# Kernel tuning notes

Measured on AMD Instinct MI355X. Metric: run time of the kernel, lower is better.

Reference implementation:

```python
import jax, jax.numpy as jnp
import numpy as np

B, T, D = 2, 2048, 1024
H, HKV, HD = 16, 4, 64  # num_heads, num_kv_heads, head_dim
EPS = 1.1920929e-07  # torch.finfo(float32).eps, nn.RMSNorm default


def _rmsnorm(x, g):
    return x * jax.lax.rsqrt(jnp.mean(x * x, axis=-1, keepdims=True) + EPS) * g


def _ternary(w):
    # ternary quantize {-1,0,+1} with straight-through estimator
    th = jnp.mean(jnp.abs(w))
    wt = jnp.sign(w) * (jnp.abs(w) > th).astype(w.dtype)
    return w + jax.lax.stop_gradient(wt - w)


def _bitlinear(x, w, g):
    return _rmsnorm(x, g) @ _ternary(w).T


def setup_inputs() -> dict:
    key = jax.random.key(0)
    ks = jax.random.split(key, 5)
    kaiming = lambda k, shape: jax.random.normal(k, shape, jnp.float32) * np.float32(np.sqrt(2.0 / shape[1]))
    return {
        "x": jax.random.normal(ks[0], (B, T, D), jnp.float32),
        "q_w": kaiming(ks[1], (D, D)),
        "q_g": jnp.ones((D,), jnp.float32),
        "k_w": kaiming(ks[2], (HKV * HD, D)),
        "k_g": jnp.ones((D,), jnp.float32),
        "v_w": kaiming(ks[3], (HKV * HD, D)),
        "o_w": kaiming(ks[4], (D, D)),
        "o_g": jnp.ones((D,), jnp.float32),
        "qk_gain": jnp.float32(5.25),
    }


def reference(x, q_w, q_g, k_w, k_g, v_w, o_w, o_g, qk_gain):
    b, t, d = x.shape
    q = _bitlinear(x, q_w, q_g).reshape(b, t, H, HD)          # [B,T,H,hd]
    k = _bitlinear(x, k_w, k_g).reshape(b, t, HKV, HD)        # [B,T,Hkv,hd]
    v = (x @ v_w.T).reshape(b, t, HKV, HD)                    # [B,T,Hkv,hd]
    rep = H // HKV
    k = jnp.repeat(k, rep, axis=2)                            # GQA expand -> [B,T,H,hd]
    v = jnp.repeat(v, rep, axis=2)
    scale = qk_gain / np.float32(np.sqrt(HD))
    attn = jnp.einsum('bqhd,bkhd->bhqk', q, k) * scale        # [B,H,T,T]
    causal = jnp.tril(jnp.ones((t, t), bool))
    attn = jnp.where(causal, attn, -jnp.inf)
    attn = jax.nn.softmax(attn, axis=-1)
    out = jnp.einsum('bhqk,bkhd->bqhd', attn, v).reshape(b, t, d)
    return _bitlinear(out, o_w, o_g)
```

## Files before the change

kernel.cpp:

```cpp
#include <hip/hip_runtime.h>
#include <hip/hip_bf16.h>
#include <cstdint>
#include <cstddef>

typedef unsigned short u16;
typedef unsigned int u32;
typedef __attribute__((ext_vector_type(8))) short short8v;
typedef __attribute__((ext_vector_type(4))) float f32x4;
typedef __attribute__((ext_vector_type(4))) u16 u16x4;
typedef __attribute__((ext_vector_type(8))) u16 u16x8;

static constexpr int Bc = 2, Tc = 2048, Dc = 1024, Hc = 16, HKVc = 4, HDc = 64;
static constexpr int Mc = Bc * Tc;
static constexpr float EPSc = 1.1920929e-07f;

static __device__ __forceinline__ u16 f2bf(float f) {
  u32 u = __builtin_bit_cast(u32, f);
  return (u16)((u + 0x7fffu + ((u >> 16) & 1u)) >> 16);
}
static __device__ __forceinline__ float bf2f(u16 b) {
  u32 u = ((u32)b) << 16;
  return __builtin_bit_cast(float, u);
}
static __device__ __forceinline__ float fast_exp2(float x) {
  float r;
  asm("v_exp_f32 %0, %1" : "=v"(r) : "v"(x));
  return r;
}
static __device__ __forceinline__ u32 cvt_pk_bf16(float lo, float hi) {
  u32 r;
  asm("v_cvt_pk_bf16_f32 %0, %1, %2" : "=v"(r) : "v"(lo), "v"(hi));
  return r;
}

__global__ __launch_bounds__(256) void np_leafsum_all(const float* __restrict__ q_w,
                                                      const float* __restrict__ k_w,
                                                      const float* __restrict__ o_w,
                                                      float* __restrict__ leaf) {
  int blk = blockIdx.x;
  const float* w;
  float* out;
  int lfbase;
  if (blk < 256)      { w = q_w; out = leaf;         lfbase = blk * 32; }
  else if (blk < 320) { w = k_w; out = leaf + 8192;  lfbase = (blk - 256) * 32; }
  else                { w = o_w; out = leaf + 10240; lfbase = (blk - 320) * 32; }
  int t = threadIdx.x;
  int lf = lfbase + (t >> 3), j = t & 7;
  const float* a = w + (size_t)lf * 128;
  float r = fabsf(a[j]);
#pragma unroll
  for (int i = 8; i < 128; i += 8) r += fabsf(a[i + j]);
  float x = r + __shfl_xor(r, 1);
  float y = x + __shfl_xor(x, 2);
  float z = y + __shfl_xor(y, 4);
  if (j == 0) out[lf] = z;
}

__global__ __launch_bounds__(256) void np_treemean3(const float* __restrict__ leaf,
                                                    float* __restrict__ th) {
  int m = blockIdx.x;
  const float* src = leaf + (m == 0 ? 0 : (m == 1 ? 8192 : 10240));
  int nle = (m == 1) ? 2048 : 8192;
  float inv_n = (m == 1) ? (1.0f / 262144.0f) : (1.0f / 1048576.0f);
  int t = threadIdx.x;
  int chunk = nle >> 8;
  float v[32];
  for (int i = 0; i < chunk; i += 4) {
    float4 f = *(const float4*)&src[t * chunk + i];
    v[i] = f.x; v[i + 1] = f.y; v[i + 2] = f.z; v[i + 3] = f.w;
  }
  for (int cnt = chunk >> 1; cnt >= 1; cnt >>= 1)
    for (int i = 0; i < cnt; ++i) v[i] = v[2 * i] + v[2 * i + 1];
  float s = v[0];
#pragma unroll
  for (int off = 1; off < 64; off <<= 1) s += __shfl_xor(s, off);
  __shared__ float red[4];
  if ((t & 63) == 0) red[t >> 6] = s;
  __syncthreads();
  if (t == 0) th[m] = ((red[0] + red[1]) + (red[2] + red[3])) * inv_n;
}

__global__ __launch_bounds__(256) void quant_split_all(const float* __restrict__ q_w,
                                                       const float* __restrict__ k_w,
                                                       const float* __restrict__ o_w,
                                                       const float* __restrict__ v_w,
                                                       const float* __restrict__ th,
                                                       u16* __restrict__ Wq,
                                                       u16* __restrict__ Wk,
                                                       u16* __restrict__ Wo,
                                                       u16* __restrict__ Vwh) {
  int i4 = blockIdx.x * 256 + threadIdx.x;
  if (i4 < 589824) {
    const float* w; u16* o; float t;
    int j;
    if (i4 < 262144)      { w = q_w; o = Wq; t = th[0]; j = i4; }
    else if (i4 < 327680) { w = k_w; o = Wk; t = th[1]; j = i4 - 262144; }
    else                  { w = o_w; o = Wo; t = th[2]; j = i4 - 327680; }
    float4 v = *(const float4*)&w[(size_t)j * 4];
    float y[4] = {v.x, v.y, v.z, v.w};
    u16x4 q;
#pragma unroll
    for (int c = 0; c < 4; ++c)
      q[c] = (y[c] > t) ? (u16)0x3F80 : ((y[c] < -t) ? (u16)0xBF80 : (u16)0);
    *(u16x4*)&o[(size_t)j * 4] = q;
  } else {
    int j = i4 - 589824;
    float4 v = *(const float4*)&v_w[(size_t)j * 4];
    float y[4] = {v.x, v.y, v.z, v.w};
    u16x4 h;
#pragma unroll
    for (int c = 0; c < 4; ++c) h[c] = f2bf(y[c]);
    *(u16x4*)&Vwh[(size_t)j * 4] = h;
  }
}

__global__ __launch_bounds__(256) void rmsnorm_split6(const float* __restrict__ X,
                                                      const float* __restrict__ g1,
                                                      const float* __restrict__ g2,
                                                      u16* __restrict__ H1, u16* __restrict__ L1,
                                                      u16* __restrict__ H2, u16* __restrict__ L2,
                                                      u16* __restrict__ HV) {
  int row = blockIdx.x;
  const float* xr = X + (size_t)row * Dc;
  int tid = threadIdx.x;
  float4 v = *(const float4*)&xr[tid * 4];
  float vv[4] = {v.x, v.y, v.z, v.w};
  if (HV != nullptr) {
    u16x4 h;
#pragma unroll
    for (int j = 0; j < 4; ++j) h[j] = f2bf(vv[j]);
    *(u16x4*)&HV[(size_t)row * Dc + tid * 4] = h;
  }
  float ss = v.x * v.x + v.y * v.y + v.z * v.z + v.w * v.w;
#pragma unroll
  for (int off = 1; off < 64; off <<= 1) ss += __shfl_xor(ss, off);
  __shared__ float red[4];
  if ((tid & 63) == 0) red[tid >> 6] = ss;
  __syncthreads();
  float tot = red[0] + red[1] + red[2] + red[3];
  float inv = 1.0f / sqrtf(tot * (1.0f / (float)Dc) + EPSc);
  {
    float4 a = *(const float4*)&g1[tid * 4];
    float ga[4] = {a.x, a.y, a.z, a.w};
    u16x4 h, l;
#pragma unroll
    for (int j = 0; j < 4; ++j) {
      float y = vv[j] * inv * ga[j];
      u16 hb = f2bf(y);
      h[j] = hb;
      l[j] = f2bf(y - bf2f(hb));
    }
    *(u16x4*)&H1[(size_t)row * Dc + tid * 4] = h;
    if (L1 != nullptr) *(u16x4*)&L1[(size_t)row * Dc + tid * 4] = l;
  }
  if (g2 != nullptr) {
    float4 a = *(const float4*)&g2[tid * 4];
    float ga[4] = {a.x, a.y, a.z, a.w};
    u16x4 h, l;
#pragma unroll
    for (int j = 0; j < 4; ++j) {
      float y = vv[j] * inv * ga[j];
      u16 hb = f2bf(y);
      h[j] = hb;
      l[j] = f2bf(y - bf2f(hb));
    }
    *(u16x4*)&H2[(size_t)row * Dc + tid * 4] = h;
    if (L2 != nullptr) *(u16x4*)&L2[(size_t)row * Dc + tid * 4] = l;
  }
}

template <bool PA, bool PB, int MODE, int MF, int NF>
__global__ __launch_bounds__(256, 1) void gemm_mfma(
    const u16* __restrict__ Ah, const u16* __restrict__ Al,
    const u16* __restrict__ Bh, const u16* __restrict__ Bl,
    int M, int N, int K,
    float* __restrict__ C, u16* __restrict__ O1, u16* __restrict__ O2) {
  constexpr int BM = MF * 32, BN = NF * 32;
  constexpr int APT = BM / 32;
  constexpr int BPT = BN / 32;
  __shared__ __align__(16) u16 AhS[BM * 64];
  __shared__ __align__(16) u16 AlS[PA ? BM * 64 : 8];
  __shared__ __align__(16) u16 BhS[BN * 64];
  __shared__ __align__(16) u16 BlS[PB ? BN * 64 : 8];
  int tid = threadIdx.x;
  int l = tid & 63, w = tid >> 6;
  int wm = (w >> 1) * (BM / 2), wn = (w & 1) * (BN / 2);
  int bm = blockIdx.y * BM, bn = blockIdx.x * BN;
  u16x8 rAh[APT], rAl[PA ? APT : 1], rBh[BPT], rBl[PB ? BPT : 1];
  f32x4 acc[MF][NF] = {};
#define LOADTILE(kb_)                                                               \
  {                                                                                 \
    _Pragma("unroll") for (int p = 0; p < APT; ++p) {                               \
      int idx = tid + p * 256;                                                      \
      int row = idx >> 3, cc = idx & 7;                                             \
      rAh[p] = *(const u16x8*)&Ah[(size_t)(bm + row) * K + (kb_) + cc * 8];         \
      if (PA) rAl[p] = *(const u16x8*)&Al[(size_t)(bm + row) * K + (kb_) + cc * 8]; \
    }                                                                               \
    _Pragma("unroll") for (int p = 0; p < BPT; ++p) {                               \
      int idx = tid + p * 256;                                                      \
      int row = idx >> 3, cc = idx & 7;                                             \
      rBh[p] = *(const u16x8*)&Bh[(size_t)(bn + row) * K + (kb_) + cc * 8];         \
      if (PB) rBl[p] = *(const u16x8*)&Bl[(size_t)(bn + row) * K + (kb_) + cc * 8]; \
    }                                                                               \
  }
  LOADTILE(0)
  for (int kb = 0; kb < K; kb += 64) {
    __syncthreads();
#pragma unroll
    for (int p = 0; p < APT; ++p) {
      int idx = tid + p * 256;
      int row = idx >> 3, cc = idx & 7;
      int off = row * 64 + ((cc * 8) ^ ((row & 7) << 3));
      *(u16x8*)&AhS[off] = rAh[p];
      if (PA) *(u16x8*)&AlS[off] = rAl[p];
    }
#pragma unroll
    for (int p = 0; p < BPT; ++p) {
      int idx = tid + p * 256;
      int row = idx >> 3, cc = idx & 7;
      int off = row * 64 + ((cc * 8) ^ ((row & 7) << 3));
      *(u16x8*)&BhS[off] = rBh[p];
      if (PB) *(u16x8*)&BlS[off] = rBl[p];
    }
    if (kb + 64 < K) LOADTILE(kb + 64)
    __syncthreads();
    __builtin_amdgcn_s_setprio(1);
#pragma unroll
    for (int sl = 0; sl < 2; ++sl) {
      short8v fa[MF], fal[MF], fb[NF], fbl[NF];
      int kof = (l >> 4) * 8 + sl * 32;
#pragma unroll
      for (int m = 0; m < MF; ++m) {
        int row = wm + m * 16 + (l & 15);
        int off = row * 64 + (kof ^ ((row & 7) << 3));
        fa[m] = *(const short8v*)&AhS[off];
        if (PA) fal[m] = *(const short8v*)&AlS[off];
      }
#pragma unroll
      for (int n = 0; n < NF; ++n) {
        int row = wn + n * 16 + (l & 15);
        int off = row * 64 + (kof ^ ((row & 7) << 3));
        fb[n] = *(const short8v*)&BhS[off];
        if (PB) fbl[n] = *(const short8v*)&BlS[off];
      }
#pragma unroll
      for (int m = 0; m < MF; ++m)
#pragma unroll
        for (int n = 0; n < NF; ++n) {
          acc[m][n] = __builtin_amdgcn_mfma_f32_16x16x32_bf16(fa[m], fb[n], acc[m][n], 0, 0, 0);
          if (PA)
            acc[m][n] = __builtin_amdgcn_mfma_f32_16x16x32_bf16(fal[m], fb[n], acc[m][n], 0, 0, 0);
          if (PB)
            acc[m][n] = __builtin_amdgcn_mfma_f32_16x16x32_bf16(fa[m], fbl[n], acc[m][n], 0, 0, 0);
        }
    }
    __builtin_amdgcn_s_setprio(0);
  }
#undef LOADTILE
#pragma unroll
  for (int m = 0; m < MF; ++m)
#pragma unroll
    for (int n = 0; n < NF; ++n)
#pragma unroll
      for (int r = 0; r < 4; ++r) {
        int grow = bm + wm + m * 16 + (l >> 4) * 4 + r;
        int gcol = bn + wn + n * 16 + (l & 15);
        float v = acc[m][n][r];
        if (MODE == 0) {
          C[(size_t)grow * N + gcol] = v;
        } else if (MODE == 1) {
          u16 hb = f2bf(v);
          O1[(size_t)grow * N + gcol] = hb;
          O2[(size_t)grow * N + gcol] = f2bf(v - bf2f(hb));
        } else {
          int k = gcol & 31;
          int gp = (gcol & ~31) | (((k >> 2) & 3) << 3) |
                   (((k >> 4) & 1) << 2) | (k & 3);
          O1[(size_t)grow * N + gp] = f2bf(v);
        }
      }
}

__global__ __launch_bounds__(256, 2) void attn_mfma8(
    const u16* __restrict__ Qh, const u16* __restrict__ Ql,
    const u16* __restrict__ Kh, const u16* __restrict__ Kl,
    const u16* __restrict__ Vt,
    const float* __restrict__ qk_gain,
    float* __restrict__ AO) {
  __shared__ __align__(16) u16 SM[24576];
  int tid = threadIdx.x;
  int w = tid >> 6, l = tid & 63;
  int pr = blockIdx.x;
  int h = blockIdx.y, b = blockIdx.z;
  int kvh = h >> 2;
  const float sc2 = qk_gain[0] * 0.125f * 1.44269504f;
  u16x8 pk[2], pl[2], pv[2];
#define AISSUE3(K0)                                                             \
  {                                                                             \
    _Pragma("unroll") for (int p = 0; p < 2; ++p) {                             \
      int idx = tid + p * 256;                                                  \
      int jj = idx >> 3, cc = idx & 7;                                          \
      size_t kb = ((size_t)(b * Tc + (K0) + jj)) * (HKVc * HDc) + kvh * 64 + cc * 8; \
      pk[p] = *(const u16x8*)&Kh[kb];                                           \
      pl[p] = *(const u16x8*)&Kl[kb];                                           \
      size_t vb = ((size_t)(kvh * 64 + jj)) * (size_t)Mc + b * Tc + (K0) + cc * 8; \
      pv[p] = *(const u16x8*)&Vt[vb];                                           \
    }                                                                           \
  }
#define WRITEBUF(BI)                                                            \
  {                                                                             \
    u16* bb = SM + (BI) * 12288;                                                \
    _Pragma("unroll") for (int p = 0; p < 2; ++p) {                             \
      int idx = tid + p * 256;                                                  \
      int jj = idx >> 3, cc = idx & 7;                                          \
      int sw = jj * 64 + ((cc * 8) ^ ((jj & 7) << 3));                          \
      *(u16x8*)&bb[sw] = pk[p];                                                 \
      *(u16x8*)&bb[4096 + sw] = pl[p];                                          \
      *(u16x8*)&bb[8192 + sw] = pv[p];                                          \
    }                                                                           \
  }
  for (int pass = 0; pass < 2; ++pass) {
    int qt = pass == 0 ? (31 - pr) : pr;
    int q0 = qt * 64;
    short8v qb_h[2], qb_l[2];
    {
      size_t qrow = (size_t)(b * Tc + q0 + w * 16 + (l & 15));
#pragma unroll
      for (int sl = 0; sl < 2; ++sl) {
        int dstart = (l >> 4) * 8 + sl * 32;
        qb_h[sl] = *(const short8v*)&Qh[qrow * Dc + h * 64 + dstart];
        qb_l[sl] = *(const short8v*)&Ql[qrow * Dc + h * 64 + dstart];
      }
    }
    f32x4 Oacc[4] = {{0,0,0,0},{0,0,0,0},{0,0,0,0},{0,0,0,0}};
    float mrow = -3.0e38f, lrow = 0.0f;
    int qmax_w = q0 + w * 16 + 15;
    int qg = q0 + w * 16 + (l & 15);
    int nsteps = qt + 1;
    AISSUE3(0)
    __syncthreads();
    WRITEBUF(0)
    if (nsteps > 1) AISSUE3(64)
    __syncthreads();
    for (int stp = 0; stp < nsteps; ++stp) {
      int k0 = stp * 64;
      u16* Kh_s = SM + (stp & 1) * 12288;
      u16* Kl_s = Kh_s + 4096;
      u16* Vt_s = Kh_s + 8192;
      if (stp + 1 < nsteps) WRITEBUF((stp + 1) & 1)
      if (stp + 2 < nsteps) AISSUE3((stp + 2) * 64)
      if (k0 <= qmax_w) {
        f32x4 s[4] = {{0,0,0,0},{0,0,0,0},{0,0,0,0},{0,0,0,0}};
        __builtin_amdgcn_s_setprio(1);
#pragma unroll
        for (int kt = 0; kt < 4; ++kt) {
          int key = kt * 16 + (l & 15);
#pragma unroll
          for (int sl = 0; sl < 2; ++sl) {
            int dstart = ((l >> 4) * 8 + 32 * sl) ^ ((key & 7) << 3);
            short8v bh = *(const short8v*)&Kh_s[key * 64 + dstart];
            short8v bl = *(const short8v*)&Kl_s[key * 64 + dstart];
            s[kt] = __builtin_amdgcn_mfma_f32_16x16x32_bf16(bh, qb_h[sl], s[kt], 0, 0, 0);
            s[kt] = __builtin_amdgcn_mfma_f32_16x16x32_bf16(bl, qb_h[sl], s[kt], 0, 0, 0);
            s[kt] = __builtin_amdgcn_mfma_f32_16x16x32_bf16(bh, qb_l[sl], s[kt], 0, 0, 0);
          }
        }
        __builtin_amdgcn_s_setprio(0);
        bool full = (k0 + 63) <= (q0 + w * 16);
        if (!full) {
#pragma unroll
          for (int kt = 0; kt < 4; ++kt)
#pragma unroll
            for (int r = 0; r < 4; ++r)
              if (k0 + kt * 16 + ((l >> 4) << 2) + r > qg) s[kt][r] = -3.0e38f;
        }
        float mk[4];
#pragma unroll
        for (int kt = 0; kt < 4; ++kt)
          mk[kt] = fmaxf(fmaxf(s[kt][0], s[kt][1]), fmaxf(s[kt][2], s[kt][3]));
        float mx = fmaxf(fmaxf(mk[0], mk[1]), fmaxf(mk[2], mk[3]));
        mx = fmaxf(mx, __shfl_xor(mx, 16));
        mx = fmaxf(mx, __shfl_xor(mx, 32));
        float mnew = fmaxf(mrow, mx);
        float msc = mnew * sc2;
        float corr = fast_exp2(__builtin_fmaf(mrow, sc2, -msc));
        mrow = mnew;
        float p[4][4];
        float sk[4];
#pragma unroll
        for (int kt = 0; kt < 4; ++kt) {
#pragma unroll
          for (int r = 0; r < 4; ++r)
            p[kt][r] = fast_exp2(__builtin_fmaf(s[kt][r], sc2, -msc));
          sk[kt] = (p[kt][0] + p[kt][1]) + (p[kt][2] + p[kt][3]);
        }
        float rs = (sk[0] + sk[1]) + (sk[2] + sk[3]);
        rs += __shfl_xor(rs, 16);
        rs += __shfl_xor(rs, 32);
        lrow = lrow * corr + rs;
#pragma unroll
        for (int dt = 0; dt < 4; ++dt) Oacc[dt] *= corr;
        short8v fbv[2];
#pragma unroll
        for (int sl = 0; sl < 2; ++sl) {
          union { u32 u[4]; short8v v; } fq;
          fq.u[0] = cvt_pk_bf16(p[2 * sl][0], p[2 * sl][1]);
          fq.u[1] = cvt_pk_bf16(p[2 * sl][2], p[2 * sl][3]);
          fq.u[2] = cvt_pk_bf16(p[2 * sl + 1][0], p[2 * sl + 1][1]);
          fq.u[3] = cvt_pk_bf16(p[2 * sl + 1][2], p[2 * sl + 1][3]);
          fbv[sl] = fq.v;
        }
        __builtin_amdgcn_s_setprio(1);
#pragma unroll
        for (int dt = 0; dt < 4; ++dt) {
          int d = dt * 16 + (l & 15);
#pragma unroll
          for (int sl = 0; sl < 2; ++sl) {
            int kstart = ((l >> 4) * 8 + 32 * sl) ^ ((d & 7) << 3);
            short8v fav = *(const short8v*)&Vt_s[d * 64 + kstart];
            Oacc[dt] = __builtin_amdgcn_mfma_f32_16x16x32_bf16(fav, fbv[sl], Oacc[dt], 0, 0, 0);
          }
        }
        __builtin_amdgcn_s_setprio(0);
      }
      __syncthreads();
    }
    float* Es = (float*)SM + w * (16 * 68);
    float invl = 1.0f / lrow;
#pragma unroll
    for (int dt = 0; dt < 4; ++dt)
#pragma unroll
      for (int r = 0; r < 4; ++r)
        Es[(l & 15) * 68 + dt * 16 + ((l >> 4) << 2) + r] = Oacc[dt][r] * invl;
    size_t arow = ((size_t)(b * Tc + q0 + w * 16 + (l >> 2))) * Dc + h * 64 + (l & 3) * 4;
#pragma unroll
    for (int j = 0; j < 4; ++j) {
      float4 vv = *(const float4*)&Es[(l >> 2) * 68 + (l & 3) * 4 + j * 16];
      *(float4*)&AO[arow + j * 16] = vv;
    }
  }
#undef AISSUE3
#undef WRITEBUF
}

extern "C" void kernel_launch(void* const* d_in, const int* in_sizes, int n_in,
                              void* d_out, int out_size, void* d_ws, size_t ws_size,
                              hipStream_t stream) {
  const float* x    = (const float*)d_in[0];
  const float* q_w  = (const float*)d_in[1];
  const float* q_g  = (const float*)d_in[2];
  const float* k_w  = (const float*)d_in[3];
  const float* k_g  = (const float*)d_in[4];
  const float* v_w  = (const float*)d_in[5];
  const float* o_w  = (const float*)d_in[6];
  const float* o_g  = (const float*)d_in[7];
  const float* qk_g = (const float*)d_in[8];

  char* base = (char*)d_ws;
  u16* Xqh = (u16*)(base + (0ull  << 20));
  u16* Xql = (u16*)(base + (8ull  << 20));
  u16* Xkh = (u16*)(base + (16ull << 20));
  u16* Xkl = (u16*)(base + (24ull << 20));
  u16* Xvh = (u16*)(base + (32ull << 20));
  u16* Xvl = (u16*)(base + (40ull << 20));
  u16* Kh  = (u16*)(base + (48ull << 20));
  u16* Kl  = (u16*)(base + (50ull << 20));
  u16* Vt  = (u16*)(base + (52ull << 20));
  u16* Wq  = (u16*)(base + (54ull << 20));
  u16* Wk  = (u16*)(base + (56ull << 20));
  u16* Wo  = (u16*)(base + (57ull << 20));
  u16* Vwh = (u16*)(base + (59ull << 20));
  float* leaf = (float*)(base + (61ull << 20));
  float* th   = leaf + 18432;
  float* AO  = (float*)base;
  u16* Xoh = Xkh;
  u16* Qh  = Xvh; u16* Ql  = Xvl;

  np_leafsum_all<<<576, 256, 0, stream>>>(q_w, k_w, o_w, leaf);
  np_treemean3<<<3, 256, 0, stream>>>(leaf, th);

  quant_split_all<<<2560, 256, 0, stream>>>(q_w, k_w, o_w, v_w, th, Wq, Wk, Wo, Vwh);

  rmsnorm_split6<<<Mc, 256, 0, stream>>>(x, q_g, k_g, Xqh, Xql, Xkh, Xkl, Xvh);

  gemm_mfma<false, false, 3, 2, 2><<<dim3(64, 4), 256, 0, stream>>>(
      Vwh, nullptr, Xvh, nullptr, 256, Mc, 1024, nullptr, Vt, nullptr);
  gemm_mfma<true, false, 1, 2, 4><<<dim3(8, 64), 256, 0, stream>>>(
      Xqh, Xql, Wq, nullptr, Mc, 1024, 1024, nullptr, Qh, Ql);
  gemm_mfma<true, false, 1, 2, 2><<<dim3(4, 64), 256, 0, stream>>>(
      Xkh, Xkl, Wk, nullptr, Mc, 256, 1024, nullptr, Kh, Kl);

  attn_mfma8<<<dim3(16, Hc, Bc), 256, 0, stream>>>(Qh, Ql, Kh, Kl, Vt, qk_g, AO);

  rmsnorm_split6<<<Mc, 256, 0, stream>>>(AO, o_g, nullptr, Xoh, nullptr, nullptr, nullptr,
                                         nullptr);
  gemm_mfma<false, false, 0, 2, 4><<<dim3(8, 64), 256, 0, stream>>>(
      Xoh, nullptr, Wo, nullptr, Mc, 1024, 1024, (float*)d_out, nullptr, nullptr);
}
```

Before: 151.7 us.

## Enlarge attention query tile to 128 rows, reusing each K/V tile across two query groups

The attention kernel now has each wave own 32 query rows (two 16-row groups), giving 128 queries per block, where it used to own 16. Each K/V tile loaded into shared memory feeds twice as many MFMAs, which halves K/V global and LDS traffic per query. The paired front/back query-tile loop inside one block is replaced by a grid ordering that launches long causal tiles first, with head and batch packed into blockIdx.x. In exchange register pressure roughly doubles (accumulators, scores, Q fragments), the causal tail gets coarser, and the grid shrinks to 512 blocks of uneven size.

```diff
diff --git a/kernel.cpp b/kernel.cpp
--- a/kernel.cpp
+++ b/kernel.cpp
@@ -281,7 +281,7 @@
       }
 }
 
-__global__ __launch_bounds__(256, 2) void attn_mfma8(
+__global__ __launch_bounds__(256, 2) void attn_mfma9(
     const u16* __restrict__ Qh, const u16* __restrict__ Ql,
     const u16* __restrict__ Kh, const u16* __restrict__ Kl,
     const u16* __restrict__ Vt,
@@ -290,8 +290,10 @@
   __shared__ __align__(16) u16 SM[24576];
   int tid = threadIdx.x;
   int w = tid >> 6, l = tid & 63;
-  int pr = blockIdx.x;
-  int h = blockIdx.y, b = blockIdx.z;
+  int h = blockIdx.x & 15, b = blockIdx.x >> 4;
+  int by = blockIdx.y;
+  int qt = (by < 8) ? (15 - by) : (by - 8);
+  int q0 = qt * 128;
   int kvh = h >> 2;
   const float sc2 = qk_gain[0] * 0.125f * 1.44269504f;
   u16x8 pk[2], pl[2], pv[2];
@@ -319,120 +321,136 @@
       *(u16x8*)&bb[8192 + sw] = pv[p];                                          \
     }                                                                           \
   }
-  for (int pass = 0; pass < 2; ++pass) {
-    int qt = pass == 0 ? (31 - pr) : pr;
-    int q0 = qt * 64;
-    short8v qb_h[2], qb_l[2];
-    {
-      size_t qrow = (size_t)(b * Tc + q0 + w * 16 + (l & 15));
-#pragma unroll
-      for (int sl = 0; sl < 2; ++sl) {
-        int dstart = (l >> 4) * 8 + sl * 32;
-        qb_h[sl] = *(const short8v*)&Qh[qrow * Dc + h * 64 + dstart];
-        qb_l[sl] = *(const short8v*)&Ql[qrow * Dc + h * 64 + dstart];
-      }
-    }
-    f32x4 Oacc[4] = {{0,0,0,0},{0,0,0,0},{0,0,0,0},{0,0,0,0}};
-    float mrow = -3.0e38f, lrow = 0.0f;
-    int qmax_w = q0 + w * 16 + 15;
-    int qg = q0 + w * 16 + (l & 15);
-    int nsteps = qt + 1;
-    AISSUE3(0)
-    __syncthreads();
-    WRITEBUF(0)
-    if (nsteps > 1) AISSUE3(64)
-    __syncthreads();
-    for (int stp = 0; stp < nsteps; ++stp) {
-      int k0 = stp * 64;
-      u16* Kh_s = SM + (stp & 1) * 12288;
-      u16* Kl_s = Kh_s + 4096;
-      u16* Vt_s = Kh_s + 8192;
-      if (stp + 1 < nsteps) WRITEBUF((stp + 1) & 1)
-      if (stp + 2 < nsteps) AISSUE3((stp + 2) * 64)
-      if (k0 <= qmax_w) {
-        f32x4 s[4] = {{0,0,0,0},{0,0,0,0},{0,0,0,0},{0,0,0,0}};
-        __builtin_amdgcn_s_setprio(1);
-#pragma unroll
-        for (int kt = 0; kt < 4; ++kt) {
-          int key = kt * 16 + (l & 15);
-#pragma unroll
-          for (int sl = 0; sl < 2; ++sl) {
-            int dstart = ((l >> 4) * 8 + 32 * sl) ^ ((key & 7) << 3);
-            short8v bh = *(const short8v*)&Kh_s[key * 64 + dstart];
-            short8v bl = *(const short8v*)&Kl_s[key * 64 + dstart];
-            s[kt] = __builtin_amdgcn_mfma_f32_16x16x32_bf16(bh, qb_h[sl], s[kt], 0, 0, 0);
-            s[kt] = __builtin_amdgcn_mfma_f32_16x16x32_bf16(bl, qb_h[sl], s[kt], 0, 0, 0);
-            s[kt] = __builtin_amdgcn_mfma_f32_16x16x32_bf16(bh, qb_l[sl], s[kt], 0, 0, 0);
+  short8v qb_h[4], qb_l[4];
+#pragma unroll
+  for (int qp = 0; qp < 2; ++qp) {
+    size_t qrow = (size_t)(b * Tc + q0 + w * 32 + qp * 16 + (l & 15));
+#pragma unroll
+    for (int sl = 0; sl < 2; ++sl) {
+      int dstart = (l >> 4) * 8 + sl * 32;
+      qb_h[qp * 2 + sl] = *(const short8v*)&Qh[qrow * Dc + h * 64 + dstart];
+      qb_l[qp * 2 + sl] = *(const short8v*)&Ql[qrow * Dc + h * 64 + dstart];
+    }
+  }
+  f32x4 Oacc[8] = {{0,0,0,0},{0,0,0,0},{0,0,0,0},{0,0,0,0},
+                   {0,0,0,0},{0,0,0,0},{0,0,0,0},{0,0,0,0}};
+  float mrow[2] = {-3.0e38f, -3.0e38f};
+  float lrow[2] = {0.f, 0.f};
+  int qmax_w = q0 + w * 32 + 31;
+  int nsteps = 2 * qt + 2;
+  AISSUE3(0)
+  WRITEBUF(0)
+  AISSUE3(64)
+  __syncthreads();
+  for (int stp = 0; stp < nsteps; ++stp) {
+    int k0 = stp * 64;
+    u16* Kh_s = SM + (stp & 1) * 12288;
+    u16* Kl_s = Kh_s + 4096;
+    u16* Vt_s = Kh_s + 8192;
+    if (stp + 1 < nsteps) WRITEBUF((stp + 1) & 1)
+    if (stp + 2 < nsteps) AISSUE3((stp + 2) * 64)
+    if (k0 <= qmax_w) {
+      f32x4 s[8] = {{0,0,0,0},{0,0,0,0},{0,0,0,0},{0,0,0,0},
+                    {0,0,0,0},{0,0,0,0},{0,0,0,0},{0,0,0,0}};
+      __builtin_amdgcn_s_setprio(1);
+#pragma unroll
+      for (int kt = 0; kt < 4; ++kt) {
+        int key = kt * 16 + (l & 15);
+#pragma unroll
+        for (int sl = 0; sl < 2; ++sl) {
+          int dstart = ((l >> 4) * 8 + 32 * sl) ^ ((key & 7) << 3);
+          short8v bh = *(const short8v*)&Kh_s[key * 64 + dstart];
+          short8v bl = *(const short8v*)&Kl_s[key * 64 + dstart];
+#pragma unroll
+          for (int qp = 0; qp < 2; ++qp) {
+            s[qp * 4 + kt] = __builtin_amdgcn_mfma_f32_16x16x32_bf16(bh, qb_h[qp * 2 + sl], s[qp * 4 + kt], 0, 0, 0);
+            s[qp * 4 + kt] = __builtin_amdgcn_mfma_f32_16x16x32_bf16(bl, qb_h[qp * 2 + sl], s[qp * 4 + kt], 0, 0, 0);
+            s[qp * 4 + kt] = __builtin_amdgcn_mfma_f32_16x16x32_bf16(bh, qb_l[qp * 2 + sl], s[qp * 4 + kt], 0, 0, 0);
           }
         }
-        __builtin_amdgcn_s_setprio(0);
-        bool full = (k0 + 63) <= (q0 + w * 16);
-        if (!full) {
+      }
+      __builtin_amdgcn_s_setprio(0);
+      bool full = (k0 + 63) <= (q0 + w * 32);
+      if (!full) {
+#pragma unroll
+        for (int qp = 0; qp < 2; ++qp) {
+          int qg = q0 + w * 32 + qp * 16 + (l & 15);
 #pragma unroll
           for (int kt = 0; kt < 4; ++kt)
 #pragma unroll
             for (int r = 0; r < 4; ++r)
-              if (k0 + kt * 16 + ((l >> 4) << 2) + r > qg) s[kt][r] = -3.0e38f;
-        }
+              if (k0 + kt * 16 + ((l >> 4) << 2) + r > qg) s[qp * 4 + kt][r] = -3.0e38f;
+        }
+      }
+      float p[2][4][4];
+#pragma unroll
+      for (int qp = 0; qp < 2; ++qp) {
         float mk[4];
 #pragma unroll
         for (int kt = 0; kt < 4; ++kt)
-          mk[kt] = fmaxf(fmaxf(s[kt][0], s[kt][1]), fmaxf(s[kt][2], s[kt][3]));
+          mk[kt] = fmaxf(fmaxf(s[qp * 4 + kt][0], s[qp * 4 + kt][1]),
+                         fmaxf(s[qp * 4 + kt][2], s[qp * 4 + kt][3]));
         float mx = fmaxf(fmaxf(mk[0], mk[1]), fmaxf(mk[2], mk[3]));
         mx = fmaxf(mx, __shfl_xor(mx, 16));
         mx = fmaxf(mx, __shfl_xor(mx, 32));
-        float mnew = fmaxf(mrow, mx);
+        float mnew = fmaxf(mrow[qp], mx);
         float msc = mnew * sc2;
-        float corr = fast_exp2(__builtin_fmaf(mrow, sc2, -msc));
-        mrow = mnew;
-        float p[4][4];
+        float corr = fast_exp2(__builtin_fmaf(mrow[qp], sc2, -msc));
+        mrow[qp] = mnew;
         float sk[4];
 #pragma unroll
         for (int kt = 0; kt < 4; ++kt) {
 #pragma unroll
           for (int r = 0; r < 4; ++r)
-            p[kt][r] = fast_exp2(__builtin_fmaf(s[kt][r], sc2, -msc));
-          sk[kt] = (p[kt][0] + p[kt][1]) + (p[kt][2] + p[kt][3]);
+            p[qp][kt][r] = fast_exp2(__builtin_fmaf(s[qp * 4 + kt][r], sc2, -msc));
+          sk[kt] = (p[qp][kt][0] + p[qp][kt][1]) + (p[qp][kt][2] + p[qp][kt][3]);
         }
         float rs = (sk[0] + sk[1]) + (sk[2] + sk[3]);
         rs += __shfl_xor(rs, 16);
         rs += __shfl_xor(rs, 32);
-        lrow = lrow * corr + rs;
-#pragma unroll
-        for (int dt = 0; dt < 4; ++dt) Oacc[dt] *= corr;
-        short8v fbv[2];
+        lrow[qp] = lrow[qp] * corr + rs;
+#pragma unroll
+        for (int dt = 0; dt < 4; ++dt) Oacc[qp * 4 + dt] *= corr;
+      }
+      short8v fbv[4];
+#pragma unroll
+      for (int qp = 0; qp < 2; ++qp)
 #pragma unroll
         for (int sl = 0; sl < 2; ++sl) {
           union { u32 u[4]; short8v v; } fq;
-          fq.u[0] = cvt_pk_bf16(p[2 * sl][0], p[2 * sl][1]);
-          fq.u[1] = cvt_pk_bf16(p[2 * sl][2], p[2 * sl][3]);
-          fq.u[2] = cvt_pk_bf16(p[2 * sl + 1][0], p[2 * sl + 1][1]);
-          fq.u[3] = cvt_pk_bf16(p[2 * sl + 1][2], p[2 * sl + 1][3]);
-          fbv[sl] = fq.v;
-        }
-        __builtin_amdgcn_s_setprio(1);
-#pragma unroll
-        for (int dt = 0; dt < 4; ++dt) {
-          int d = dt * 16 + (l & 15);
-#pragma unroll
-          for (int sl = 0; sl < 2; ++sl) {
-            int kstart = ((l >> 4) * 8 + 32 * sl) ^ ((d & 7) << 3);
-            short8v fav = *(const short8v*)&Vt_s[d * 64 + kstart];
-            Oacc[dt] = __builtin_amdgcn_mfma_f32_16x16x32_bf16(fav, fbv[sl], Oacc[dt], 0, 0, 0);
-          }
-        }
-        __builtin_amdgcn_s_setprio(0);
-      }
-      __syncthreads();
-    }
-    float* Es = (float*)SM + w * (16 * 68);
-    float invl = 1.0f / lrow;
+          fq.u[0] = cvt_pk_bf16(p[qp][2 * sl][0], p[qp][2 * sl][1]);
+          fq.u[1] = cvt_pk_bf16(p[qp][2 * sl][2], p[qp][2 * sl][3]);
+          fq.u[2] = cvt_pk_bf16(p[qp][2 * sl + 1][0], p[qp][2 * sl + 1][1]);
+          fq.u[3] = cvt_pk_bf16(p[qp][2 * sl + 1][2], p[qp][2 * sl + 1][3]);
+          fbv[qp * 2 + sl] = fq.v;
+        }
+      __builtin_amdgcn_s_setprio(1);
+#pragma unroll
+      for (int dt = 0; dt < 4; ++dt) {
+        int d = dt * 16 + (l & 15);
+#pragma unroll
+        for (int sl = 0; sl < 2; ++sl) {
+          int kstart = ((l >> 4) * 8 + 32 * sl) ^ ((d & 7) << 3);
+          short8v fav = *(const short8v*)&Vt_s[d * 64 + kstart];
+#pragma unroll
+          for (int qp = 0; qp < 2; ++qp)
+            Oacc[qp * 4 + dt] = __builtin_amdgcn_mfma_f32_16x16x32_bf16(fav, fbv[qp * 2 + sl], Oacc[qp * 4 + dt], 0, 0, 0);
+        }
+      }
+      __builtin_amdgcn_s_setprio(0);
+    }
+    __syncthreads();
+  }
+  float* Es = (float*)SM + w * (16 * 68);
+#pragma unroll
+  for (int qp = 0; qp < 2; ++qp) {
+    float invl = 1.0f / lrow[qp];
 #pragma unroll
     for (int dt = 0; dt < 4; ++dt)
 #pragma unroll
       for (int r = 0; r < 4; ++r)
-        Es[(l & 15) * 68 + dt * 16 + ((l >> 4) << 2) + r] = Oacc[dt][r] * invl;
-    size_t arow = ((size_t)(b * Tc + q0 + w * 16 + (l >> 2))) * Dc + h * 64 + (l & 3) * 4;
+        Es[(l & 15) * 68 + dt * 16 + ((l >> 4) << 2) + r] = Oacc[qp * 4 + dt][r] * invl;
+    size_t arow = ((size_t)(b * Tc + q0 + w * 32 + qp * 16 + (l >> 2))) * Dc + h * 64 + (l & 3) * 4;
 #pragma unroll
     for (int j = 0; j < 4; ++j) {
       float4 vv = *(const float4*)&Es[(l >> 2) * 68 + (l & 3) * 4 + j * 16];
@@ -490,7 +508,7 @@
   gemm_mfma<true, false, 1, 2, 2><<<dim3(4, 64), 256, 0, stream>>>(
       Xkh, Xkl, Wk, nullptr, Mc, 256, 1024, nullptr, Kh, Kl);
 
-  attn_mfma8<<<dim3(16, Hc, Bc), 256, 0, stream>>>(Qh, Ql, Kh, Kl, Vt, qk_g, AO);
+  attn_mfma9<<<dim3(32, 16, 1), 256, 0, stream>>>(Qh, Ql, Kh, Kl, Vt, qk_g, AO);
 
   rmsnorm_split6<<<Mc, 256, 0, stream>>>(AO, o_g, nullptr, Xoh, nullptr, nullptr, nullptr,
                                          nullptr);
```

After: 149.7 us. No clear change (-1.3%).
